# Kernel optimization log

Hardware: AMD Instinct MI355X
Metric: run time of the kernel (lower is better)

The kernel has to match this reference:

```python
import jax, jax.numpy as jnp
import numpy as np
import math

L = 2          # gnn_num_layers
NDIM = 256     # gnn_hidden_size
H = 8          # num_heads
HH = H // 2    # heads per (full, local) split
DK = NDIM // H # 32, also == edim (relation_share_heads)
EDIM = DK
B, NPB = 32, 128
N = B * NPB            # 4096 nodes
EF = B * NPB * NPB     # 524288 complete-graph edges
EL = 131072            # local-graph edges
ELG = 262144           # line-graph edges
R = 128                # relation vocab


def _ln(x, g, b, eps=1e-5):
    m = x.mean(-1, keepdims=True)
    v = ((x - m) ** 2).mean(-1, keepdims=True)
    return (x - m) / jnp.sqrt(v + eps) * g + b


def _ffn(x, W1, b1, W2, b2, g, b):
    h = jax.nn.relu(x @ W1 + b1)
    return _ln(x + h @ W2 + b2, g, b)


def _edge_attn(q, k, v, e, src, dst, n_seg):
    """Relation-aware graph attention (DGL propagate_attention + edge_softmax).
    q,k,v: [n_seg,h,d]; e: [E,h,d] edge-relation bias or None; src,dst: [E].
    score_e = ((k[src]+e) . q[dst]) / sqrt(d); softmax over in-edges of dst;
    out[dst] = sum alpha_e * (v[src]+e)."""
    ks = k[src] + e if e is not None else k[src]          # [E,h,d]
    vs = v[src] + e if e is not None else v[src]          # [E,h,d]
    s = jnp.einsum('ehd,ehd->eh', ks, q[dst]) / math.sqrt(q.shape[-1])
    smax = jax.ops.segment_max(s, dst, num_segments=n_seg)
    ex = jnp.exp(s - jnp.maximum(smax, -1e30)[dst])
    den = jax.ops.segment_sum(ex, dst, num_segments=n_seg)[dst]
    alpha = ex / jnp.where(den > 0, den, 1.0)
    return jax.ops.segment_sum(alpha[..., None] * vs, dst, num_segments=n_seg)


def _model(x, rel_embed,
           n_Wq, n_bq, n_Wk, n_bk, n_Wv, n_bv, n_Wo, n_bo, n_ln_g, n_ln_b,
           n_f_W1, n_f_b1, n_f_W2, n_f_b2, n_f_ln_g, n_f_ln_b,
           e_Wsrc, e_Wdst, e_Wq, e_bq, e_Wk, e_Wv, e_Wo, e_bo, e_ln_g, e_ln_b,
           e_f_W1, e_f_b1, e_f_W2, e_f_b2, e_f_ln_g, e_f_ln_b,
           full_src, full_dst, g_src, g_dst, lg_src, lg_dst, edge_feat, full_edge_feat):
    lg_x = rel_embed[edge_feat]            # [EL, EDIM]  (shared embedding)
    lg_x_full = rel_embed[full_edge_feat]  # [EF, EDIM]  (fixed across layers)
    n, el, ef = x.shape[0], lg_x.shape[0], lg_x_full.shape[0]
    for i in range(L):
        # ---------- node update: first HH heads on full graph, last HH on local ----------
        q = (x @ n_Wq[i] + n_bq[i]).reshape(n, H, DK)
        k = (x @ n_Wk[i] + n_bk[i]).reshape(n, H, DK)
        v = (x @ n_Wv[i] + n_bv[i]).reshape(n, H, DK)
        # edim == d_k -> relation bias broadcast across heads (the expand branch)
        e_full = jnp.broadcast_to(lg_x_full[:, None, :], (ef, HH, DK))
        e_loc = jnp.broadcast_to(lg_x[:, None, :], (el, HH, DK))
        o1 = _edge_attn(q[:, :HH], k[:, :HH], v[:, :HH], e_full, full_src, full_dst, n)
        o2 = _edge_attn(q[:, HH:], k[:, HH:], v[:, HH:], e_loc, g_src, g_dst, n)
        o = jnp.concatenate([o1, o2], axis=1).reshape(n, NDIM)
        x_new = _ln(x + o @ n_Wo[i] + n_bo[i], n_ln_g[i], n_ln_b[i])
        x_new = _ffn(x_new, n_f_W1[i], n_f_b1[i], n_f_W2[i], n_f_b2[i], n_f_ln_g[i], n_f_ln_b[i])
        # ---------- edge update on line graph, conditioned on PRE-update src/dst node feats ----------
        mixed = lg_x + x[g_src] @ e_Wsrc[i] + x[g_dst] @ e_Wdst[i]  # [EL, EDIM]
        dke = EDIM // H
        eq = (mixed @ e_Wq[i] + e_bq[i]).reshape(el, H, dke)
        ek = (mixed @ e_Wk[i]).reshape(el, H, dke)
        ev = (mixed @ e_Wv[i]).reshape(el, H, dke)
        ow = _edge_attn(eq, ek, ev, None, lg_src, lg_dst, el).reshape(el, EDIM)
        lg_new = _ln(lg_x + ow @ e_Wo[i] + e_bo[i], e_ln_g[i], e_ln_b[i])
        lg_new = _ffn(lg_new, e_f_W1[i], e_f_b1[i], e_f_W2[i], e_f_b2[i], e_f_ln_g[i], e_f_ln_b[i])
        x, lg_x = x_new, lg_new
    return x, lg_x


def setup_inputs() -> dict:
    key = jax.random.key(0)
    ki = iter(jax.random.split(key, 48))
    def p(shape, scale=0.05):
        return jax.random.normal(next(ki), shape, dtype=jnp.float32) * scale
    rng = np.random.default_rng(0)
    blk = (np.arange(B, dtype=np.int32) * NPB)
    ii, jj = np.meshgrid(np.arange(NPB, dtype=np.int32), np.arange(NPB, dtype=np.int32), indexing='ij')
    full_src = (blk[:, None, None] + ii[None]).reshape(-1)   # block-diagonal complete graph
    full_dst = (blk[:, None, None] + jj[None]).reshape(-1)
    epb = EL // B
    g_src = (np.repeat(blk, epb) + rng.integers(0, NPB, EL)).astype(np.int32)
    g_dst = (np.repeat(blk, epb) + rng.integers(0, NPB, EL)).astype(np.int32)
    lpb = ELG // B
    eblk = np.arange(B, dtype=np.int32) * epb
    lg_src = (np.repeat(eblk, lpb) + rng.integers(0, epb, ELG)).astype(np.int32)
    lg_dst = (np.repeat(eblk, lpb) + rng.integers(0, epb, ELG)).astype(np.int32)
    return dict(
        x=jax.random.normal(next(ki), (N, NDIM), dtype=jnp.float32),
        rel_embed=p((R, EDIM), 1.0),
        full_src=jnp.asarray(full_src), full_dst=jnp.asarray(full_dst),
        g_src=jnp.asarray(g_src), g_dst=jnp.asarray(g_dst),
        lg_src=jnp.asarray(lg_src), lg_dst=jnp.asarray(lg_dst),
        edge_feat=jnp.asarray(rng.integers(0, R, EL).astype(np.int32)),
        full_edge_feat=jnp.asarray(rng.integers(0, R, EF).astype(np.int32)),
        n_Wq=p((L, NDIM, NDIM)), n_bq=p((L, NDIM)),
        n_Wk=p((L, NDIM, NDIM)), n_bk=p((L, NDIM)),
        n_Wv=p((L, NDIM, NDIM)), n_bv=p((L, NDIM)),
        n_Wo=p((L, NDIM, NDIM)), n_bo=p((L, NDIM)),
        n_ln_g=jnp.ones((L, NDIM), jnp.float32), n_ln_b=jnp.zeros((L, NDIM), jnp.float32),
        n_f_W1=p((L, NDIM, 4 * NDIM)), n_f_b1=p((L, 4 * NDIM)),
        n_f_W2=p((L, 4 * NDIM, NDIM)), n_f_b2=p((L, NDIM)),
        n_f_ln_g=jnp.ones((L, NDIM), jnp.float32), n_f_ln_b=jnp.zeros((L, NDIM), jnp.float32),
        e_Wsrc=p((L, NDIM, EDIM)), e_Wdst=p((L, NDIM, EDIM)),
        e_Wq=p((L, EDIM, EDIM)), e_bq=p((L, EDIM)),
        e_Wk=p((L, EDIM, EDIM)), e_Wv=p((L, EDIM, EDIM)),
        e_Wo=p((L, EDIM, EDIM)), e_bo=p((L, EDIM)),
        e_ln_g=jnp.ones((L, EDIM), jnp.float32), e_ln_b=jnp.zeros((L, EDIM), jnp.float32),
        e_f_W1=p((L, EDIM, 4 * EDIM)), e_f_b1=p((L, 4 * EDIM)),
        e_f_W2=p((L, 4 * EDIM, EDIM)), e_f_b2=p((L, EDIM)),
        e_f_ln_g=jnp.ones((L, EDIM), jnp.float32), e_f_ln_b=jnp.zeros((L, EDIM), jnp.float32),
    )


def reference(x, rel_embed, full_src, full_dst, g_src, g_dst, lg_src, lg_dst,
              edge_feat, full_edge_feat,
              n_Wq, n_bq, n_Wk, n_bk, n_Wv, n_bv, n_Wo, n_bo, n_ln_g, n_ln_b,
              n_f_W1, n_f_b1, n_f_W2, n_f_b2, n_f_ln_g, n_f_ln_b,
              e_Wsrc, e_Wdst, e_Wq, e_bq, e_Wk, e_Wv, e_Wo, e_bo, e_ln_g, e_ln_b,
              e_f_W1, e_f_b1, e_f_W2, e_f_b2, e_f_ln_g, e_f_ln_b):
    return _model(x, rel_embed,
                  n_Wq, n_bq, n_Wk, n_bk, n_Wv, n_bv, n_Wo, n_bo, n_ln_g, n_ln_b,
                  n_f_W1, n_f_b1, n_f_W2, n_f_b2, n_f_ln_g, n_f_ln_b,
                  e_Wsrc, e_Wdst, e_Wq, e_bq, e_Wk, e_Wv, e_Wo, e_bo, e_ln_g, e_ln_b,
                  e_f_W1, e_f_b1, e_f_W2, e_f_b2, e_f_ln_g, e_f_ln_b,
                  full_src, full_dst, g_src, g_dst, lg_src, lg_dst, edge_feat, full_edge_feat)
```

## Files before the change

kernel.cpp:

```cpp
#include <hip/hip_runtime.h>
#include <hip/hip_bf16.h>

typedef __hip_bfloat16 bf16;
typedef unsigned short ush;

static constexpr int kN   = 4096;
static constexpr int kND  = 256;
static constexpr int kEL  = 131072;
static constexpr int kED  = 32;
static constexpr int kELG = 262144;
static constexpr int kL   = 2;
static constexpr int kQW  = 832;
static constexpr int kKV  = 512;
static constexpr float kScaleN = 0.17677669529663687f;

using frag_ab = __attribute__((ext_vector_type(8))) short;
using frag_cd = __attribute__((ext_vector_type(4))) float;

__device__ __forceinline__ float ldf(const void* p, size_t i, int isbf){
    return isbf ? __bfloat162float(((const bf16*)p)[i]) : ((const float*)p)[i];
}
__device__ __forceinline__ ush f2b(float f){ bf16 h = __float2bfloat16(f); return *(ush*)&h; }
__device__ __forceinline__ float b2f(ush u){ return __uint_as_float(((unsigned)u)<<16); }
__device__ __forceinline__ ush ldb(const void* p, size_t i, int isbf){
    return isbf ? ((const ush*)p)[i] : f2b(((const float*)p)[i]);
}

__global__ void detect_k(const ush* __restrict__ xin, int* __restrict__ flag){
    const int t = threadIdx.x;
    int pl = 0;
    for (int i = t; i < 128; i += 64) {
        ush u = xin[i];
        int e = (u >> 7) & 0xFF;
        if (e == 0 || (e >= 110 && e <= 140)) ++pl;
    }
    #pragma unroll
    for (int off = 32; off > 0; off >>= 1) pl += __shfl_down(pl, off);
    if (t == 0) *flag = (pl >= 102) ? 1 : 0;
}

__global__ void setup_misc_k(const void* __restrict__ xin, const void* __restrict__ rel,
                             const int* __restrict__ feat,
                             const void* __restrict__ bq, const void* __restrict__ bk,
                             const void* __restrict__ bv,
                             float* __restrict__ xA, ush* __restrict__ xAb,
                             ush* __restrict__ lgA,
                             float* __restrict__ bQKV,
                             int* __restrict__ cntL, int* __restrict__ cntG,
                             const int* __restrict__ flag){
    const int isbf = *flag;
    long g = (long)blockIdx.x*256 + threadIdx.x;
    if (g < (long)kN*kND) {
        float v = ldf(xin, g, isbf);
        xA[g] = v; xAb[g] = f2b(v);
        return;
    }
    g -= (long)kN*kND;
    if (g < (long)kEL*kED) { int e = (int)(g >> 5), d = (int)(g & 31);
        lgA[g] = ldb(rel, (size_t)feat[e]*kED + d, isbf); return; }
    g -= (long)kEL*kED;
    if (g < 2*kQW) {
        int layer = (int)(g / kQW), j = (int)(g - (long)layer*kQW);
        float v = 0.f;
        if (j < 768) { int w = j >> 8, jj = j & 255;
            const void* B = (w==0)?bq:((w==1)?bk:bv);
            v = ldf(B, (size_t)layer*256 + jj, isbf); }
        bQKV[g] = v; return;
    }
    g -= 2*kQW;
    if (g < kN) { cntL[g] = 0; return; }
    g -= kN;
    if (g < kEL) { cntG[g] = 0; return; }
}

__global__ __launch_bounds__(256) void trans_tiled_k(
    const void* __restrict__ nWq, const void* __restrict__ nWk, const void* __restrict__ nWv,
    const void* __restrict__ nWo, const void* __restrict__ nF1, const void* __restrict__ nF2,
    const void* __restrict__ eWs, const void* __restrict__ eWd,
    const void* __restrict__ eWq, const void* __restrict__ eWk, const void* __restrict__ eWv,
    const void* __restrict__ eWo, const void* __restrict__ eF1, const void* __restrict__ eF2,
    const int* __restrict__ flag,
    ush* __restrict__ wtQKVSD, ush* __restrict__ wtO, ush* __restrict__ wtF1,
    ush* __restrict__ wtF2, ush* __restrict__ wtEQKV, ush* __restrict__ wtEO,
    ush* __restrict__ wtEF1, ush* __restrict__ wtEF2)
{
    __shared__ ush lds[32][33];
    const int isbf = *flag;
    int idx = blockIdx.x;
    const void* src; size_t soff; ush* dstp; size_t doff;
    int Ns, Kd, r0, c0;
    if (idx < 384) {
        int w = idx >> 7, rem = idx & 127;
        int layer = rem >> 6, tile = rem & 63;
        r0 = (tile >> 3) << 5; c0 = (tile & 7) << 5;
        src = (w==0)?nWq:((w==1)?nWk:nWv); soff = (size_t)layer*65536;
        Ns = 256; Kd = 256;
        dstp = wtQKVSD; doff = (size_t)layer*212992 + (size_t)w*65536;
    } else if ((idx -= 384) < 32) {
        int w = idx >> 4, rem = idx & 15;
        int layer = rem >> 3, tile = rem & 7;
        r0 = tile << 5; c0 = 0;
        src = w ? eWd : eWs; soff = (size_t)layer*8192;
        Ns = 32; Kd = 256;
        dstp = wtQKVSD; doff = (size_t)layer*212992 + (size_t)(768 + w*32)*256;
    } else if ((idx -= 32) < 128) {
        int layer = idx >> 6, tile = idx & 63;
        r0 = (tile >> 3) << 5; c0 = (tile & 7) << 5;
        src = nWo; soff = (size_t)layer*65536; Ns = 256; Kd = 256;
        dstp = wtO; doff = (size_t)layer*65536;
    } else if ((idx -= 128) < 512) {
        int layer = idx >> 8, tile = idx & 255;
        r0 = (tile >> 5) << 5; c0 = (tile & 31) << 5;
        src = nF1; soff = (size_t)layer*262144; Ns = 1024; Kd = 256;
        dstp = wtF1; doff = (size_t)layer*262144;
    } else if ((idx -= 512) < 512) {
        int layer = idx >> 8, tile = idx & 255;
        r0 = (tile >> 3) << 5; c0 = (tile & 7) << 5;
        src = nF2; soff = (size_t)layer*262144; Ns = 256; Kd = 1024;
        dstp = wtF2; doff = (size_t)layer*262144;
    } else if ((idx -= 512) < 6) {
        int w = idx >> 1, layer = idx & 1;
        r0 = 0; c0 = 0;
        src = (w==0)?eWq:((w==1)?eWk:eWv); soff = (size_t)layer*1024; Ns = 32; Kd = 32;
        dstp = wtEQKV; doff = (size_t)(w*2 + layer)*1024;
    } else if ((idx -= 6) < 2) {
        r0 = 0; c0 = 0;
        src = eWo; soff = (size_t)idx*1024; Ns = 32; Kd = 32;
        dstp = wtEO; doff = (size_t)idx*1024;
    } else if ((idx -= 2) < 8) {
        int layer = idx >> 2, tile = idx & 3;
        r0 = 0; c0 = tile << 5;
        src = eF1; soff = (size_t)layer*4096; Ns = 128; Kd = 32;
        dstp = wtEF1; doff = (size_t)layer*4096;
    } else {
        idx -= 8;
        int layer = idx >> 2, tile = idx & 3;
        r0 = tile << 5; c0 = 0;
        src = eF2; soff = (size_t)layer*4096; Ns = 32; Kd = 128;
        dstp = wtEF2; doff = (size_t)layer*4096;
    }
    const int t = threadIdx.x;
    const int c = t & 31, rb = t >> 5;
    #pragma unroll
    for (int p = 0; p < 4; ++p) {
        int r = rb + p*8;
        lds[r][c] = ldb(src, soff + (size_t)(r0 + r)*Ns + c0 + c, isbf);
    }
    __syncthreads();
    #pragma unroll
    for (int p = 0; p < 4; ++p) {
        int rr = rb + p*8;
        dstp[doff + (size_t)(c0 + rr)*Kd + r0 + c] = lds[c][rr];
    }
}

__global__ void count2_k(const int* __restrict__ gd, const int* __restrict__ lgd,
                         int* __restrict__ cntL, int* __restrict__ cntG){
    int g = blockIdx.x*256 + threadIdx.x;
    if (g < kEL) atomicAdd(&cntL[gd[g]], 1);
    else if (g < kEL + kELG) atomicAdd(&cntG[lgd[g - kEL]], 1);
}
__global__ __launch_bounds__(256) void scan_blk2_k(
    const int* __restrict__ cntL, const int* __restrict__ cntG,
    int* __restrict__ rowL, int* __restrict__ rowG, int* __restrict__ bsum)
{
    __shared__ int s[256];
    const int t = threadIdx.x;
    const bool isL = blockIdx.x < 4;
    const int* cnt = isL ? cntL : cntG;
    int* out = isL ? rowL : rowG;
    const int blk = isL ? blockIdx.x : blockIdx.x - 4;
    const int n = isL ? kN : kEL;
    const int b0 = blk*1024;
    int v[4], pre[4], tsum = 0;
    #pragma unroll
    for (int j=0;j<4;++j){
        int idx = b0 + t*4 + j;
        v[j] = (idx < n) ? cnt[idx] : 0;
        pre[j] = tsum; tsum += v[j];
    }
    s[t] = tsum; __syncthreads();
    for (int off=1; off<256; off<<=1){
        int x = (t>=off) ? s[t-off] : 0;
        __syncthreads();
        s[t] += x;
        __syncthreads();
    }
    int texc = s[t] - tsum;
    #pragma unroll
    for (int j=0;j<4;++j){
        int idx = b0 + t*4 + j;
        if (idx < n) out[idx] = texc + pre[j];
    }
    if (t == 255) bsum[(isL ? 0 : 8) + blk] = s[255];
}
__global__ __launch_bounds__(256) void scan_top2_k(int* __restrict__ bsum){
    __shared__ int sL[256], sG[256];
    const int t = threadIdx.x;
    int vL = (t < 4)   ? bsum[t]     : 0;
    int vG = (t < 128) ? bsum[8 + t] : 0;
    sL[t] = vL; sG[t] = vG; __syncthreads();
    for (int off=1; off<256; off<<=1){
        int xL = (t>=off) ? sL[t-off] : 0;
        int xG = (t>=off) ? sG[t-off] : 0;
        __syncthreads();
        sL[t] += xL; sG[t] += xG;
        __syncthreads();
    }
    if (t < 4)   bsum[t]     = sL[t] - vL;
    if (t < 128) bsum[8 + t] = sG[t] - vG;
}
__global__ void scan_add2_k(int* __restrict__ rowL, int* __restrict__ rowG,
                            const int* __restrict__ bsum,
                            int* __restrict__ curL, int* __restrict__ curG){
    int g = blockIdx.x*256 + threadIdx.x;
    if (g < kN){ int v = rowL[g] + bsum[g >> 10]; rowL[g] = v; curL[g] = v; }
    else if (g < kN + kEL){ int gg = g - kN;
        int v = rowG[gg] + bsum[8 + (gg >> 10)]; rowG[gg] = v; curG[gg] = v; }
    if (g == 0){ rowL[kN] = kEL; rowG[kEL] = kELG; }
}
__global__ void fill2_k(const int* __restrict__ gd, const int* __restrict__ lgd,
                        int* __restrict__ curL, int* __restrict__ curG,
                        int* __restrict__ eidL, int* __restrict__ eidG){
    int g = blockIdx.x*256 + threadIdx.x;
    if (g < kEL){ int pos = atomicAdd(&curL[gd[g]], 1); eidL[pos] = g; }
    else if (g < kEL + kELG){ int gg = g - kEL;
        int pos = atomicAdd(&curG[lgd[gg]], 1); eidG[pos] = gg; }
}

__global__ __launch_bounds__(256) void mgemm_k(
    const float* __restrict__ A, const ush* __restrict__ WT,
    const void* __restrict__ bias, size_t boff,
    float* __restrict__ C, const int* __restrict__ flag,
    int M, int N, int K, int flags, ush* __restrict__ aux, ush* __restrict__ aux2)
{
    __shared__ __align__(16) ush As[64*72];
    __shared__ __align__(16) ush Ws[64*72];
    const int isbf = *flag;
    const int t = threadIdx.x;
    const int m0 = blockIdx.y*64, n0 = blockIdx.x*64;
    const int wave = t>>6, lane = t&63;
    const int quad = lane>>4, l15 = lane&15;
    const int r = t>>3, kq = (t&7)*8;
    const bool abf = flags & 32;
    const bool spk = flags & 128;
    const int Kc   = spk ? (K / gridDim.z) : K;
    const int koff = spk ? (blockIdx.z * Kc) : 0;

    frag_cd acc[4];
    #pragma unroll
    for (int tl=0; tl<4; ++tl)
        #pragma unroll
        for (int j=0;j<4;++j) acc[tl][j] = 0.f;

    const float* ap0 = A + (size_t)(m0+r)*K + koff + kq;
    const float* ap1 = A + (size_t)(m0+r+32)*K + koff + kq;
    const ush*   ab0 = (const ush*)A + (size_t)(m0+r)*K + koff + kq;
    const ush*   ab1 = (const ush*)A + (size_t)(m0+r+32)*K + koff + kq;
    const ush*   wp0 = WT + (size_t)(n0+r)*K + koff + kq;
    const ush*   wp1 = WT + (size_t)(n0+r+32)*K + koff + kq;

    float4 a00,a01,a10,a11; uint4 av0,av1, wv0,wv1;
    auto loadT = [&](int kk){
        if (abf) { av0 = *(const uint4*)(ab0+kk); av1 = *(const uint4*)(ab1+kk); }
        else { a00 = *(const float4*)(ap0+kk); a01 = *(const float4*)(ap0+kk+4);
               a10 = *(const float4*)(ap1+kk); a11 = *(const float4*)(ap1+kk+4); }
        wv0 = *(const uint4*)(wp0+kk); wv1 = *(const uint4*)(wp1+kk);
    };
    loadT(0);

    for (int kk = 0; kk < Kc; kk += 64) {
        if (abf) {
            *(uint4*)&As[r*72 + kq]        = av0;
            *(uint4*)&As[(r+32)*72 + kq]   = av1;
        } else {
            *(ushort4*)&As[r*72 + kq]       = make_ushort4(f2b(a00.x),f2b(a00.y),f2b(a00.z),f2b(a00.w));
            *(ushort4*)&As[r*72 + kq + 4]   = make_ushort4(f2b(a01.x),f2b(a01.y),f2b(a01.z),f2b(a01.w));
            *(ushort4*)&As[(r+32)*72 + kq]     = make_ushort4(f2b(a10.x),f2b(a10.y),f2b(a10.z),f2b(a10.w));
            *(ushort4*)&As[(r+32)*72 + kq + 4] = make_ushort4(f2b(a11.x),f2b(a11.y),f2b(a11.z),f2b(a11.w));
        }
        *(uint4*)&Ws[r*72 + kq]      = wv0;
        *(uint4*)&Ws[(r+32)*72 + kq] = wv1;
        __syncthreads();
        if (kk + 64 < Kc) loadT(kk + 64);
        frag_ab af0 = *(const frag_ab*)&As[(wave*16 + l15)*72 + quad*8];
        frag_ab af1 = *(const frag_ab*)&As[(wave*16 + l15)*72 + 32 + quad*8];
        #pragma unroll
        for (int tl = 0; tl < 4; ++tl) {
            frag_ab bf0 = *(const frag_ab*)&Ws[(tl*16 + l15)*72 + quad*8];
            acc[tl] = __builtin_amdgcn_mfma_f32_16x16x32_bf16(af0, bf0, acc[tl], 0, 0, 0);
            frag_ab bf1 = *(const frag_ab*)&Ws[(tl*16 + l15)*72 + 32 + quad*8];
            acc[tl] = __builtin_amdgcn_mfma_f32_16x16x32_bf16(af1, bf1, acc[tl], 0, 0, 0);
        }
        __syncthreads();
    }
    const bool do_relu = flags & 2;
    const bool has_b   = (flags & 4) && (!spk || blockIdx.z == 0);
    const bool obf     = flags & 8;
    float* Cz = spk ? (C + (size_t)blockIdx.z * M * N) : C;
    #pragma unroll
    for (int tl = 0; tl < 4; ++tl) {
        int col = n0 + tl*16 + l15;
        float bv = 0.f;
        if (has_b) bv = (flags & 16) ? ((const float*)bias)[boff + col]
                                     : ldf(bias, boff + col, isbf);
        int adst = -1; bool tox = false;
        if (flags & 64 && col >= 256) {
            int c = col - 256;
            if (c < 512) {
                int isv = c >> 8;
                int cc = c & 255;
                int h = cc >> 5, d = cc & 31;
                int base = (h < 4) ? h*64 : 256 + (h-4)*64;
                adst = base + isv*32 + d;
            } else { adst = c - 512; tox = true; }
        }
        #pragma unroll
        for (int rg = 0; rg < 4; ++rg) {
            int row = m0 + wave*16 + quad*4 + rg;
            float v = acc[tl][rg] + bv;
            if (do_relu) v = fmaxf(v, 0.f);
            if (flags & 64) {
                if (col < 256)  C[(size_t)row*256 + col] = v;
                else if (tox)   aux2[(size_t)row*64 + adst] = f2b(v);
                else            aux[(size_t)row*kKV + adst] = f2b(v);
            } else if (obf) ((ush*)C)[(size_t)row*N + col] = f2b(v);
            else            Cz[(size_t)row*N + col] = v;
        }
    }
}

__global__ __launch_bounds__(256) void ln_k(
    const float* __restrict__ a, const float* __restrict__ b, const float* __restrict__ b2,
    const void* __restrict__ g, const void* __restrict__ be, size_t goff,
    float* __restrict__ out, ush* __restrict__ outb,
    const int* __restrict__ flag, int D)
{
    const int isbf = *flag;
    const int row = blockIdx.x*4 + (threadIdx.x >> 6);
    const int t = threadIdx.x & 63;
    float v[4];
    int cnt = 0;
    float s = 0.f;
    for (int i = t; i < D; i += 64) {
        float x = a[(size_t)row*D + i];
        if (b)  x += b[(size_t)row*D + i];
        if (b2) x += b2[(size_t)row*D + i];
        v[cnt++] = x; s += x;
    }
    #pragma unroll
    for (int off = 32; off > 0; off >>= 1) s += __shfl_down(s, off);
    s = __shfl(s, 0);
    const float mean = s / D;
    float qq = 0.f;
    for (int c2 = 0; c2 < cnt; ++c2) { float d = v[c2]-mean; qq += d*d; }
    #pragma unroll
    for (int off = 32; off > 0; off >>= 1) qq += __shfl_down(qq, off);
    qq = __shfl(qq, 0);
    const float inv = rsqrtf(fmaxf(qq, 0.f) / D + 1e-5f);
    cnt = 0;
    for (int i = t; i < D; i += 64) {
        float r = (v[cnt++] - mean)*inv*ldf(g, goff + i, isbf) + ldf(be, goff + i, isbf);
        out[(size_t)row*D + i] = r;
        outb[(size_t)row*D + i] = f2b(r);
    }
}

__global__ __launch_bounds__(256) void eqkv_mfma_k(
    const ush* __restrict__ lg, const ush* __restrict__ xsd,
    const int* __restrict__ gsrc, const int* __restrict__ gdst,
    const ush* __restrict__ WQKV, size_t woff,
    const void* __restrict__ bq, size_t boff,
    ush* __restrict__ eq, ush* __restrict__ ekv,
    const int* __restrict__ flag)
{
    __shared__ __align__(16) ush mixs[128*40];
    __shared__ __align__(16) ush wts[3][32*40];
    __shared__ float bqs[32];
    const int isbf = *flag;
    const int t = threadIdx.x;
    const int e0 = blockIdx.x * 128;
    #pragma unroll
    for (int i = t; i < 768; i += 256) {
        int m = i >> 8, r2 = i & 255;
        int n = r2 >> 3, k4 = (r2 & 7) * 4;
        *(ushort4*)&wts[m][n*40 + k4] =
            *(const ushort4*)&WQKV[(size_t)m*2048 + woff + (size_t)n*32 + k4];
    }
    if (t < 32) bqs[t] = ldf(bq, boff + t, isbf);
    {
        int r = t >> 1, c0 = (t & 1) * 16;
        int e = e0 + r;
        int s = gsrc[e], d2 = gdst[e];
        const ush* lp = lg  + (size_t)e*32  + c0;
        const ush* sp = xsd + (size_t)s*64  + c0;
        const ush* dp = xsd + (size_t)d2*64 + 32 + c0;
        uint4 lv0 = *(const uint4*)lp,     lv1 = *(const uint4*)(lp+8);
        uint4 sv0 = *(const uint4*)sp,     sv1 = *(const uint4*)(sp+8);
        uint4 dv0 = *(const uint4*)dp,     dv1 = *(const uint4*)(dp+8);
        auto pk = [](unsigned a, unsigned b, unsigned c)->unsigned {
            ush lo = f2b(b2f((ush)(a & 0xffff)) + b2f((ush)(b & 0xffff)) + b2f((ush)(c & 0xffff)));
            ush hi = f2b(b2f((ush)(a >> 16))    + b2f((ush)(b >> 16))    + b2f((ush)(c >> 16)));
            return (unsigned)lo | ((unsigned)hi << 16);
        };
        uint4 o0, o1;
        o0.x = pk(lv0.x, sv0.x, dv0.x); o0.y = pk(lv0.y, sv0.y, dv0.y);
        o0.z = pk(lv0.z, sv0.z, dv0.z); o0.w = pk(lv0.w, sv0.w, dv0.w);
        o1.x = pk(lv1.x, sv1.x, dv1.x); o1.y = pk(lv1.y, sv1.y, dv1.y);
        o1.z = pk(lv1.z, sv1.z, dv1.z); o1.w = pk(lv1.w, sv1.w, dv1.w);
        *(uint4*)&mixs[r*40 + c0]     = o0;
        *(uint4*)&mixs[r*40 + c0 + 8] = o1;
    }
    __syncthreads();
    const int wave = t >> 6, l15 = t & 15, quad = (t >> 4) & 3;
    #pragma unroll
    for (int mi = 0; mi < 2; ++mi) {
        const int mt = wave*2 + mi;
        frag_ab af = *(const frag_ab*)&mixs[(mt*16 + l15)*40 + quad*8];
        #pragma unroll
        for (int w = 0; w < 3; ++w) {
            #pragma unroll
            for (int nt = 0; nt < 2; ++nt) {
                frag_ab bf = *(const frag_ab*)&wts[w][(nt*16 + l15)*40 + quad*8];
                frag_cd acc = {0.f, 0.f, 0.f, 0.f};
                acc = __builtin_amdgcn_mfma_f32_16x16x32_bf16(af, bf, acc, 0, 0, 0);
                const float bv = (w==0) ? bqs[nt*16 + l15] : 0.f;
                const int col = nt*16 + l15;
                const int h = col >> 2, d = col & 3;
                #pragma unroll
                for (int rg = 0; rg < 4; ++rg) {
                    int row = e0 + mt*16 + quad*4 + rg;
                    float v = acc[rg] + bv;
                    if (w == 0)      eq[(size_t)row*32 + col] = f2b(v);
                    else if (w == 1) ekv[(size_t)row*64 + h*8 + d] = f2b(v);
                    else             ekv[(size_t)row*64 + h*8 + 4 + d] = f2b(v);
                }
            }
        }
    }
}

__global__ __launch_bounds__(256) void effn_mfma_k(
    const ush* __restrict__ A,
    const ush* __restrict__ W1T, size_t w1off, const void* __restrict__ b1, size_t b1off,
    const ush* __restrict__ W2T, size_t w2off, const void* __restrict__ b2, size_t b2off,
    const void* __restrict__ g, const void* __restrict__ be, size_t goff,
    ush* __restrict__ out, const int* __restrict__ flag)
{
    __shared__ __align__(16) ush w1t[128*40];
    __shared__ __align__(16) ush w2t[32*136];
    __shared__ __align__(16) ush hid[64*136];
    __shared__ float b1s[128], b2s[32];
    const int isbf = *flag;
    const int t = threadIdx.x;
    const int wave = t >> 6, l15 = t & 15, quad = (t >> 4) & 3;

    #pragma unroll
    for (int i = t; i < 1024; i += 256) {
        int n1 = i >> 3, k4 = (i & 7) * 4;
        *(ushort4*)&w1t[n1*40 + k4] = *(const ushort4*)&W1T[w1off + (size_t)n1*32 + k4];
        int n2 = i >> 5, kq2 = (i & 31) * 4;
        *(ushort4*)&w2t[n2*136 + kq2] = *(const ushort4*)&W2T[w2off + (size_t)n2*128 + kq2];
    }
    if (t < 128) b1s[t] = ldf(b1, b1off + t, isbf);
    if (t < 32)  b2s[t] = ldf(b2, b2off + t, isbf);
    __syncthreads();

    const float g0  = ldf(g,  goff + l15, isbf),      g1v = ldf(g,  goff + 16 + l15, isbf);
    const float be0 = ldf(be, goff + l15, isbf),      be1 = ldf(be, goff + 16 + l15, isbf);
    const float bb0 = b2s[l15], bb1 = b2s[16 + l15];

    for (int tt = 0; tt < 2; ++tt) {
        const int e0 = (blockIdx.x*2 + tt) * 64;
        {
            const int m = wave*16 + l15;
            frag_ab af = *(const frag_ab*)&A[(size_t)(e0+m)*32 + quad*8];
            #pragma unroll
            for (int nt = 0; nt < 8; ++nt) {
                frag_ab bf = *(const frag_ab*)&w1t[(nt*16 + l15)*40 + quad*8];
                frag_cd acc = {0.f, 0.f, 0.f, 0.f};
                acc = __builtin_amdgcn_mfma_f32_16x16x32_bf16(af, bf, acc, 0, 0, 0);
                float bv = b1s[nt*16 + l15];
                #pragma unroll
                for (int rg = 0; rg < 4; ++rg) {
                    int row = wave*16 + quad*4 + rg;
                    hid[row*136 + nt*16 + l15] = f2b(fmaxf(acc[rg] + bv, 0.f));
                }
            }
        }
        frag_cd acc2[2] = {{0.f,0.f,0.f,0.f},{0.f,0.f,0.f,0.f}};
        #pragma unroll
        for (int ks = 0; ks < 4; ++ks) {
            frag_ab af2 = *(const frag_ab*)&hid[(wave*16 + l15)*136 + ks*32 + quad*8];
            #pragma unroll
            for (int tl = 0; tl < 2; ++tl) {
                frag_ab bf2 = *(const frag_ab*)&w2t[(tl*16 + l15)*136 + ks*32 + quad*8];
                acc2[tl] = __builtin_amdgcn_mfma_f32_16x16x32_bf16(af2, bf2, acc2[tl], 0, 0, 0);
            }
        }
        #pragma unroll
        for (int rg = 0; rg < 4; ++rg) {
            const int row = e0 + wave*16 + quad*4 + rg;
            float v0 = acc2[0][rg] + bb0 + b2f(A[(size_t)row*32 + l15]);
            float v1 = acc2[1][rg] + bb1 + b2f(A[(size_t)row*32 + 16 + l15]);
            float s = v0 + v1;
            s += __shfl_xor(s,1); s += __shfl_xor(s,2); s += __shfl_xor(s,4); s += __shfl_xor(s,8);
            const float mean = s * (1.f/32.f);
            float q = (v0-mean)*(v0-mean) + (v1-mean)*(v1-mean);
            q += __shfl_xor(q,1); q += __shfl_xor(q,2); q += __shfl_xor(q,4); q += __shfl_xor(q,8);
            const float inv = rsqrtf(q * (1.f/32.f) + 1e-5f);
            out[(size_t)row*32 + l15]      = f2b((v0-mean)*inv*g0  + be0);
            out[(size_t)row*32 + 16 + l15] = f2b((v1-mean)*inv*g1v + be1);
        }
    }
}

__global__ __launch_bounds__(512) void full_attn_k(
    const float* __restrict__ q, const ush* __restrict__ kv,
    const void* __restrict__ rel, const int* __restrict__ feat, ush* __restrict__ o,
    const int* __restrict__ flag)
{
    __shared__ __align__(8) ush ks[128][36];
    __shared__ __align__(8) ush vs[128][36];
    __shared__ __align__(8) ush rs[128][36];
    __shared__ float pb[8][32][34];
    const int isbf = *flag;
    const int bid = blockIdx.x;
    const int b = bid >> 4, h = (bid >> 2) & 3, qtr = bid & 3;
    const int t = threadIdx.x;
    for (int i = t; i < 4096; i += 512) {
        int r = i >> 5, d = i & 31;
        rs[r][d] = ldb(rel, i, isbf);
        const ush* kvrow = kv + (size_t)(b*128 + r)*kKV + h*64 + d;
        ks[r][d] = kvrow[0];
        vs[r][d] = kvrow[32];
    }
    __syncthreads();
    const int wave = t >> 6, lane = t & 63;
    const int dstL = lane >> 1, part = lane & 1;
    const int dst = qtr*32 + dstL;
    const int dbase = part*16;
    float qr[16];
    { size_t base = ((size_t)(b*128 + dst))*256 + h*32 + dbase;
      #pragma unroll
      for (int d=0; d<16; ++d) qr[d] = q[base + d]; }
    const int* fp = feat + (size_t)b*16384 + dst;
    const int s0 = wave*16;
    float m = -1e30f, l = 0.f;
    float acc[16];
    #pragma unroll
    for (int d=0; d<16; ++d) acc[d] = 0.f;
    int f = fp[s0*128];
    for (int sI = 0; sI < 16; ++sI) {
        const int s = s0 + sI;
        int fn = (sI+1 < 16) ? fp[(s+1)*128] : 0;
        float er[16];
        float scp = 0.f;
        #pragma unroll
        for (int j2 = 0; j2 < 4; ++j2) {
            ushort4 eu = *(const ushort4*)&rs[f][dbase + j2*4];
            ushort4 ku = *(const ushort4*)&ks[s][dbase + j2*4];
            float e0 = b2f(eu.x), e1 = b2f(eu.y), e2 = b2f(eu.z), e3 = b2f(eu.w);
            er[j2*4+0]=e0; er[j2*4+1]=e1; er[j2*4+2]=e2; er[j2*4+3]=e3;
            scp += (b2f(ku.x)+e0)*qr[j2*4+0] + (b2f(ku.y)+e1)*qr[j2*4+1]
                 + (b2f(ku.z)+e2)*qr[j2*4+2] + (b2f(ku.w)+e3)*qr[j2*4+3];
        }
        const float sc = (scp + __shfl_xor(scp, 1)) * kScaleN;
        float mn = fmaxf(m, sc);
        float c0 = __expf(m - mn);
        float pp = __expf(sc - mn);
        l = l*c0 + pp;
        #pragma unroll
        for (int j2 = 0; j2 < 4; ++j2) {
            ushort4 vu = *(const ushort4*)&vs[s][dbase + j2*4];
            acc[j2*4+0] = acc[j2*4+0]*c0 + pp*(b2f(vu.x)+er[j2*4+0]);
            acc[j2*4+1] = acc[j2*4+1]*c0 + pp*(b2f(vu.y)+er[j2*4+1]);
            acc[j2*4+2] = acc[j2*4+2]*c0 + pp*(b2f(vu.z)+er[j2*4+2]);
            acc[j2*4+3] = acc[j2*4+3]*c0 + pp*(b2f(vu.w)+er[j2*4+3]);
        }
        m = mn; f = fn;
    }
    if (part == 0) { pb[wave][dstL][0] = m; pb[wave][dstL][1] = l; }
    #pragma unroll
    for (int d=0; d<16; ++d) pb[wave][dstL][2 + dbase + d] = acc[d];
    __syncthreads();
    {
        const int dstL2 = t & 31, grp = t >> 5;
        float mw[8], lw[8];
        #pragma unroll
        for (int w=0; w<8; ++w){ mw[w]=pb[w][dstL2][0]; lw[w]=pb[w][dstL2][1]; }
        float M = mw[0];
        #pragma unroll
        for (int w=1; w<8; ++w) M = fmaxf(M, mw[w]);
        float sw[8];
        float L = 0.f;
        #pragma unroll
        for (int w=0; w<8; ++w){ sw[w] = __expf(mw[w]-M); L += lw[w]*sw[w]; }
        const float inv = 1.f / fmaxf(L, 1e-30f);
        size_t base = ((size_t)(b*128 + qtr*32 + dstL2))*kND + h*32 + grp*2;
        #pragma unroll
        for (int d=0; d<2; ++d) {
            float a = 0.f;
            #pragma unroll
            for (int w=0; w<8; ++w) a += pb[w][dstL2][2+grp*2+d]*sw[w];
            o[base + d] = f2b(a*inv);
        }
    }
}

__global__ __launch_bounds__(256) void loc_gather_k(
    const float* __restrict__ q, const ush* __restrict__ kv,
    const ush* __restrict__ lg, const int* __restrict__ gsrc,
    const int* __restrict__ rowp, const int* __restrict__ eidl,
    ush* __restrict__ o)
{
    __shared__ int eids[192], srcs[192];
    const int n = blockIdx.x;
    const int beg = rowp[n], end = rowp[n+1];
    const int deg = end - beg;
    {
        const int tc = threadIdx.x;
        const int dc = (deg < 192) ? deg : 192;
        if (tc < dc) { int e = eidl[beg + tc]; eids[tc] = e; srcs[tc] = gsrc[e]; }
    }
    __syncthreads();
    const int h = threadIdx.x >> 6;
    const int lane = threadIdx.x & 63;
    const int g = lane >> 4;
    const int d0 = (lane & 15) * 2;
    const size_t hoff = (size_t)(4 + h) * 32 + d0;
    const float2 q2 = *(const float2*)&q[(size_t)n*256 + hoff];
    float m = -1e30f, l = 0.f, ax = 0.f, ay = 0.f;
    if (deg > 0) {
        const int nIter = (deg + 3) >> 2;
        int idx = beg + g;
        for (int it = 0; it < nIter; ++it) {
            const bool valid = idx < end;
            const int ii = min(idx, end-1) - beg;
            int e, s;
            if (ii < 192) { e = eids[ii]; s = srcs[ii]; }
            else          { e = eidl[beg + ii]; s = gsrc[e]; }
            idx += 4;
            const ushort2 ku = *(const ushort2*)&kv[(size_t)s*kKV + 256 + h*64 + d0];
            const ushort2 lvu = *(const ushort2*)&lg[(size_t)e*32 + d0];
            const ushort2 vu = *(const ushort2*)&kv[(size_t)s*kKV + 256 + h*64 + 32 + d0];
            const float lvx = b2f(lvu.x), lvy = b2f(lvu.y);
            float part = (b2f(ku.x)+lvx)*q2.x + (b2f(ku.y)+lvy)*q2.y;
            part += __shfl_xor(part, 1);
            part += __shfl_xor(part, 2);
            part += __shfl_xor(part, 4);
            part += __shfl_xor(part, 8);
            const float sc = part * kScaleN;
            const float mn = valid ? fmaxf(m, sc) : m;
            const float c  = __expf(m - mn);
            const float pp = valid ? __expf(sc - mn) : 0.f;
            l  = l*c  + pp;
            ax = ax*c + pp*(b2f(vu.x)+lvx);
            ay = ay*c + pp*(b2f(vu.y)+lvy);
            m  = mn;
        }
        #pragma unroll
        for (int off = 16; off <= 32; off <<= 1) {
            const float mo = __shfl_xor(m, off);
            const float lo = __shfl_xor(l, off);
            const float xo = __shfl_xor(ax, off);
            const float yo = __shfl_xor(ay, off);
            const float M  = fmaxf(m, mo);
            const float c1 = __expf(m - M);
            const float c2 = __expf(mo - M);
            l  = l*c1  + lo*c2;
            ax = ax*c1 + xo*c2;
            ay = ay*c1 + yo*c2;
            m  = M;
        }
    }
    if (g == 0) {
        const float inv = 1.f / fmaxf(l, 1e-30f);
        *(ushort2*)&o[(size_t)n*kND + hoff] = make_ushort2(f2b(ax*inv), f2b(ay*inv));
    }
}

__global__ __launch_bounds__(256) void lgs_ewo_k(
    const ush* __restrict__ eq, const ush* __restrict__ ekv,
    const int* __restrict__ lsrc, const int* __restrict__ rowp, const int* __restrict__ eidl,
    const ush* __restrict__ res,
    const ush* __restrict__ WO, size_t wooff, const void* __restrict__ bo, size_t booff,
    const void* __restrict__ g1, const void* __restrict__ be1, size_t g1off,
    ush* __restrict__ out, const int* __restrict__ flag)
{
    __shared__ __align__(16) ush ows[32*40];
    __shared__ __align__(16) ush wos[32*40];
    __shared__ float cs[32][36];
    __shared__ float bos[32], gs[32], bs[32];
    __shared__ int srcs[256];
    const int isbf = *flag;
    const int t = threadIdx.x;
    const int base = blockIdx.x * 32;
    {
        int n = t >> 3, k4 = (t & 7) * 4;
        *(ushort4*)&wos[n*40 + k4] = *(const ushort4*)&WO[wooff + (size_t)n*32 + k4];
    }
    if (t < 32) {
        bos[t] = ldf(bo, booff + t, isbf);
        gs[t]  = ldf(g1, g1off + t, isbf);
        bs[t]  = ldf(be1, g1off + t, isbf);
    }
    const int beg0 = rowp[base];
    {
        int cnt = rowp[base + 32] - beg0;
        if (cnt > 256) cnt = 256;
        for (int j = t; j < cnt; j += 256) srcs[j] = lsrc[eidl[beg0 + j]];
    }
    __syncthreads();
    {
        const int d2 = base + (t >> 3), h = t & 7;
        const ushort4 qu = *(const ushort4*)&eq[(size_t)d2*32 + h*4];
        const float q0 = b2f(qu.x), q1 = b2f(qu.y), q2 = b2f(qu.z), q3 = b2f(qu.w);
        const int beg = rowp[d2], end = rowp[d2+1];
        float m = -1e30f, l = 0.f;
        float4 acc = make_float4(0.f,0.f,0.f,0.f);
        for (int i = beg; i < end; ++i) {
            const int io = i - beg0;
            const int s = (io < 256) ? srcs[io] : lsrc[eidl[i]];
            const uint4 kv8 = *(const uint4*)&ekv[(size_t)s*64 + h*8];
            const ush k0 = (ush)(kv8.x & 0xffff), k1 = (ush)(kv8.x >> 16);
            const ush k2 = (ush)(kv8.y & 0xffff), k3 = (ush)(kv8.y >> 16);
            const ush v0u = (ush)(kv8.z & 0xffff), v1u = (ush)(kv8.z >> 16);
            const ush v2u = (ush)(kv8.w & 0xffff), v3u = (ush)(kv8.w >> 16);
            float sc = (b2f(k0)*q0 + b2f(k1)*q1 + b2f(k2)*q2 + b2f(k3)*q3) * 0.5f;
            float mn = fmaxf(m, sc);
            float c = __expf(m - mn);
            float pp = __expf(sc - mn);
            l = l*c + pp;
            acc.x = acc.x*c + pp*b2f(v0u);
            acc.y = acc.y*c + pp*b2f(v1u);
            acc.z = acc.z*c + pp*b2f(v2u);
            acc.w = acc.w*c + pp*b2f(v3u);
            m = mn;
        }
        const float inv = 1.f / fmaxf(l, 1e-30f);
        const int r = t >> 3, c0 = h*4;
        ows[r*40 + c0 + 0] = f2b(acc.x*inv);
        ows[r*40 + c0 + 1] = f2b(acc.y*inv);
        ows[r*40 + c0 + 2] = f2b(acc.z*inv);
        ows[r*40 + c0 + 3] = f2b(acc.w*inv);
    }
    __syncthreads();
    {
        const int wave = t >> 6, l15 = t & 15, quad = (t >> 4) & 3;
        const int mt = wave & 1, nt = wave >> 1;
        frag_ab af = *(const frag_ab*)&ows[(mt*16 + l15)*40 + quad*8];
        frag_ab bf = *(const frag_ab*)&wos[(nt*16 + l15)*40 + quad*8];
        frag_cd acc = {0.f, 0.f, 0.f, 0.f};
        acc = __builtin_amdgcn_mfma_f32_16x16x32_bf16(af, bf, acc, 0, 0, 0);
        #pragma unroll
        for (int rg = 0; rg < 4; ++rg) {
            const int row = mt*16 + quad*4 + rg;
            const int col = nt*16 + l15;
            cs[row][col] = acc[rg] + bos[col] + b2f(res[(size_t)(base+row)*32 + col]);
        }
    }
    __syncthreads();
    {
        const int row = t >> 3, c0 = (t & 7) * 4;
        const float v0 = cs[row][c0], v1 = cs[row][c0+1];
        const float v2 = cs[row][c0+2], v3 = cs[row][c0+3];
        float s = v0+v1+v2+v3;
        s += __shfl_xor(s,1); s += __shfl_xor(s,2); s += __shfl_xor(s,4);
        const float mean = s * (1.f/32.f);
        float qq = (v0-mean)*(v0-mean)+(v1-mean)*(v1-mean)
                 + (v2-mean)*(v2-mean)+(v3-mean)*(v3-mean);
        qq += __shfl_xor(qq,1); qq += __shfl_xor(qq,2); qq += __shfl_xor(qq,4);
        const float inv = rsqrtf(qq * (1.f/32.f) + 1e-5f);
        out[(size_t)(base+row)*32 + c0 + 0] = f2b((v0-mean)*inv*gs[c0+0] + bs[c0+0]);
        out[(size_t)(base+row)*32 + c0 + 1] = f2b((v1-mean)*inv*gs[c0+1] + bs[c0+1]);
        out[(size_t)(base+row)*32 + c0 + 2] = f2b((v2-mean)*inv*gs[c0+2] + bs[c0+2]);
        out[(size_t)(base+row)*32 + c0 + 3] = f2b((v3-mean)*inv*gs[c0+3] + bs[c0+3]);
    }
}

__global__ void out_k(const float* __restrict__ xf, const ush* __restrict__ lgf,
                      void* __restrict__ out, const int* __restrict__ flag){
    const int isbf = *flag;
    int g = blockIdx.x*256 + threadIdx.x;
    if (g < kN*kND) {
        float v = xf[g];
        if (isbf) ((ush*)out)[g] = f2b(v);
        else      ((float*)out)[g] = v;
    } else {
        ush u = lgf[g - kN*kND];
        if (isbf) ((ush*)out)[g] = u;
        else      ((float*)out)[g] = b2f(u);
    }
}

static inline void mgemm(const float* A, const ush* WT, const void* bias, size_t boff,
                         float* C, const int* flag, int M, int N, int K, int flags,
                         hipStream_t s, ush* aux, ush* aux2, int splitz = 1){
    dim3 grid((N+63)/64, M/64, splitz);
    mgemm_k<<<grid, 256, 0, s>>>(A, WT, bias, boff, C, flag, M, N, K, flags, aux, aux2);
}

extern "C" void kernel_launch(void* const* d_in, const int* in_sizes, int n_in,
                              void* d_out, int out_size, void* d_ws, size_t ws_size,
                              hipStream_t stream) {
    const void* x_in      = d_in[0];
    const void* rel       = d_in[1];
    const int* g_src      = (const int*)d_in[4];
    const int* g_dst      = (const int*)d_in[5];
    const int* lg_src     = (const int*)d_in[6];
    const int* lg_dst     = (const int*)d_in[7];
    const int* edge_feat  = (const int*)d_in[8];
    const int* full_feat  = (const int*)d_in[9];
    const void* n_Wq   = d_in[10];
    const void* n_bq   = d_in[11];
    const void* n_Wk   = d_in[12];
    const void* n_bk   = d_in[13];
    const void* n_Wv   = d_in[14];
    const void* n_bv   = d_in[15];
    const void* n_Wo   = d_in[16];
    const void* n_bo   = d_in[17];
    const void* n_lng  = d_in[18];
    const void* n_lnb  = d_in[19];
    const void* n_fW1  = d_in[20];
    const void* n_fb1  = d_in[21];
    const void* n_fW2  = d_in[22];
    const void* n_fb2  = d_in[23];
    const void* n_flng = d_in[24];
    const void* n_flnb = d_in[25];
    const void* e_Wsrc = d_in[26];
    const void* e_Wdst = d_in[27];
    const void* e_Wq   = d_in[28];
    const void* e_bq   = d_in[29];
    const void* e_Wk   = d_in[30];
    const void* e_Wv   = d_in[31];
    const void* e_Wo   = d_in[32];
    const void* e_bo   = d_in[33];
    const void* e_lng  = d_in[34];
    const void* e_lnb  = d_in[35];
    const void* e_fW1  = d_in[36];
    const void* e_fb1  = d_in[37];
    const void* e_fW2  = d_in[38];
    const void* e_fb2  = d_in[39];
    const void* e_flng = d_in[40];
    const void* e_flnb = d_in[41];

    float* p = (float*)d_ws;
    size_t off = 0;
    auto AL = [&](size_t n){ float* r = p + off; off += n; return r; };
    int* flagp = (int*)AL(64);
    float* xA   = AL((size_t)kN*kND);
    float* xB   = AL((size_t)kN*kND);
    float* xM   = AL((size_t)kN*kND);
    ush*   xAb  = (ush*)AL((size_t)kN*kND/2);
    ush*   xBb  = (ush*)AL((size_t)kN*kND/2);
    ush*   xMb  = (ush*)AL((size_t)kN*kND/2);
    float* qkvb = AL((size_t)kN*kND);
    ush*   kvaux= (ush*)AL((size_t)kN*kKV/2);
    ush*   xsdb = (ush*)AL((size_t)kN*32);
    ush*   ob   = (ush*)AL((size_t)kN*kND/2);
    float* tN   = AL((size_t)kN*kND*2);
    ush*   nh   = (ush*)AL((size_t)kN*512);
    ush*   lgA  = (ush*)AL((size_t)kEL*kED/2);
    ush*   lgB  = (ush*)AL((size_t)kEL*kED/2);
    ush*   lgM  = (ush*)AL((size_t)kEL*kED/2);
    ush*   eqb  = (ush*)AL((size_t)kEL*16);
    ush*   ekvb = (ush*)AL((size_t)kEL*32);
    int* cntL  = (int*)AL(kN);
    int* rowL  = (int*)AL(kN + 64);
    int* curL  = (int*)AL(kN);
    int* eidL  = (int*)AL(kEL);
    int* cntG  = (int*)AL(kEL);
    int* rowG  = (int*)AL(kEL + 64);
    int* curG  = (int*)AL(kEL);
    int* eidG  = (int*)AL(kELG);
    int* bsum  = (int*)AL(256);
    ush* wtQKVSD = (ush*)AL(212992);
    float* bQKV  = AL(2*kQW);
    ush* wtO  = (ush*)AL(65536);
    ush* wtF1 = (ush*)AL(262144);
    ush* wtF2 = (ush*)AL(262144);
    ush* wtEQKV = (ush*)AL(3072);
    ush* wtEO   = (ush*)AL(1024);
    ush* wtEF1  = (ush*)AL(4096);
    ush* wtEF2  = (ush*)AL(4096);
    if (ws_size < off * sizeof(float)) return;

    float* tN2 = tN + (size_t)kN*kND;

    detect_k<<<1, 64, 0, stream>>>((const ush*)x_in, flagp);
    {
        long total = (long)kN*kND + (long)kEL*kED + 2*kQW + kN + kEL;
        int blocks = (int)((total + 255) / 256);
        setup_misc_k<<<blocks, 256, 0, stream>>>(x_in, rel, edge_feat, n_bq, n_bk, n_bv,
                                                 xA, xAb, lgA, bQKV, cntL, cntG, flagp);
    }
    trans_tiled_k<<<1592, 256, 0, stream>>>(n_Wq, n_Wk, n_Wv, n_Wo, n_fW1, n_fW2,
                                            e_Wsrc, e_Wdst, e_Wq, e_Wk, e_Wv, e_Wo,
                                            e_fW1, e_fW2, flagp,
                                            wtQKVSD, wtO, wtF1, wtF2,
                                            wtEQKV, wtEO, wtEF1, wtEF2);

    count2_k<<<(kEL+kELG)/256, 256, 0, stream>>>(g_dst, lg_dst, cntL, cntG);
    scan_blk2_k<<<132, 256, 0, stream>>>(cntL, cntG, rowL, rowG, bsum);
    scan_top2_k<<<1, 256, 0, stream>>>(bsum);
    scan_add2_k<<<(kN+kEL)/256, 256, 0, stream>>>(rowL, rowG, bsum, curL, curG);
    fill2_k<<<(kEL+kELG)/256, 256, 0, stream>>>(g_dst, lg_dst, curL, curG, eidL, eidG);

    float* xc = xA;  float* xn = xB;
    ush* xcb = xAb;  ush* xnb = xBb;
    ush* lgc = lgA;  ush* lgn = lgB;

    for (int i = 0; i < kL; ++i) {
        const size_t o256 = (size_t)i*kND;
        const size_t o1024= (size_t)i*1024;
        const size_t o32  = (size_t)i*kED;
        const size_t o128 = (size_t)i*128;

        mgemm((const float*)xcb, wtQKVSD + (size_t)i*212992, bQKV, (size_t)i*kQW, qkvb,
              flagp, kN, kQW, kND, 4|16|32|64, stream, kvaux, xsdb);
        full_attn_k<<<512, 512, 0, stream>>>(qkvb, kvaux, rel, full_feat, ob, flagp);
        loc_gather_k<<<kN, 256, 0, stream>>>(qkvb, kvaux, lgc, g_src, rowL, eidL, ob);
        mgemm((const float*)ob, wtO + (size_t)i*65536, n_bo, o256, tN, flagp,
              kN, kND, kND, 4|32|128, stream, nullptr, nullptr, 2);
        ln_k<<<kN/4, 256, 0, stream>>>(xc, tN, tN2, n_lng, n_lnb, o256, xM, xMb, flagp, kND);
        mgemm((const float*)xMb, wtF1 + (size_t)i*262144, n_fb1, o1024, (float*)nh, flagp,
              kN, 1024, kND, 4|2|8|32, stream, nullptr, nullptr);
        mgemm((const float*)nh, wtF2 + (size_t)i*262144, n_fb2, o256, tN, flagp,
              kN, kND, 1024, 4|32|128, stream, nullptr, nullptr, 2);
        ln_k<<<kN/4, 256, 0, stream>>>(xM, tN, tN2, n_flng, n_flnb, o256, xn, xnb, flagp, kND);

        eqkv_mfma_k<<<kEL/128, 256, 0, stream>>>(lgc, xsdb, g_src, g_dst,
                                                 wtEQKV, (size_t)i*1024, e_bq, o32,
                                                 eqb, ekvb, flagp);
        lgs_ewo_k<<<kEL/32, 256, 0, stream>>>(eqb, ekvb, lg_src, rowG, eidG,
                                              lgc, wtEO, (size_t)i*1024, e_bo, o32,
                                              e_lng, e_lnb, o32, lgM, flagp);
        effn_mfma_k<<<kEL/128, 256, 0, stream>>>(lgM, wtEF1, (size_t)i*4096, e_fb1, o128,
                                                 wtEF2, (size_t)i*4096, e_fb2, o32,
                                                 e_flng, e_flnb, o32, lgn, flagp);

        { float* t = xc; xc = xn; xn = t; }
        { ush* t = xcb; xcb = xnb; xnb = t; }
        { ush* t = lgc; lgc = lgn; lgn = t; }
    }

    out_k<<<(kN*kND + kEL*kED)/256, 256, 0, stream>>>(xc, lgc, d_out, flagp);
}
```

Baseline: 513.0 us.

## Fuse output and FFN2 projections with residual-add layernorm in one MFMA kernel

Replaces the two split-K mgemm calls (output projection and FFN second linear) plus the separate layernorm kernels with a single gemm_ln_k. Each block computes a 16x256 row tile with MFMA, adds bias and the residual, then applies layernorm in-block and writes fp32 and bf16 outputs. This removes the fp32 partial-sum round trips through tN/tN2 and two launches per use. The cost is that each block now streams the whole weight matrix for only 16 rows, and the grid has just 256 blocks with no split-K, so the K=1024 case may be less parallel.

```diff
diff --git a/kernel.cpp b/kernel.cpp
--- a/kernel.cpp
+++ b/kernel.cpp
@@ -330,39 +330,102 @@
     }
 }
 
-__global__ __launch_bounds__(256) void ln_k(
-    const float* __restrict__ a, const float* __restrict__ b, const float* __restrict__ b2,
+__global__ __launch_bounds__(256) void gemm_ln_k(
+    const ush* __restrict__ A, const ush* __restrict__ WT,
+    const void* __restrict__ bias, size_t boff,
+    const float* __restrict__ res,
     const void* __restrict__ g, const void* __restrict__ be, size_t goff,
     float* __restrict__ out, ush* __restrict__ outb,
-    const int* __restrict__ flag, int D)
+    const int* __restrict__ flag, int K)
 {
+    __shared__ __align__(16) ush As[16*72];
+    __shared__ __align__(16) ush Ws[256*72];
+    __shared__ float cs[16][260];
+    __shared__ float bs[256], gsv[256], bes[256];
     const int isbf = *flag;
-    const int row = blockIdx.x*4 + (threadIdx.x >> 6);
-    const int t = threadIdx.x & 63;
-    float v[4];
-    int cnt = 0;
-    float s = 0.f;
-    for (int i = t; i < D; i += 64) {
-        float x = a[(size_t)row*D + i];
-        if (b)  x += b[(size_t)row*D + i];
-        if (b2) x += b2[(size_t)row*D + i];
-        v[cnt++] = x; s += x;
-    }
-    #pragma unroll
-    for (int off = 32; off > 0; off >>= 1) s += __shfl_down(s, off);
-    s = __shfl(s, 0);
-    const float mean = s / D;
-    float qq = 0.f;
-    for (int c2 = 0; c2 < cnt; ++c2) { float d = v[c2]-mean; qq += d*d; }
-    #pragma unroll
-    for (int off = 32; off > 0; off >>= 1) qq += __shfl_down(qq, off);
-    qq = __shfl(qq, 0);
-    const float inv = rsqrtf(fmaxf(qq, 0.f) / D + 1e-5f);
-    cnt = 0;
-    for (int i = t; i < D; i += 64) {
-        float r = (v[cnt++] - mean)*inv*ldf(g, goff + i, isbf) + ldf(be, goff + i, isbf);
-        out[(size_t)row*D + i] = r;
-        outb[(size_t)row*D + i] = f2b(r);
+    const int t = threadIdx.x;
+    const int m0 = blockIdx.x * 16;
+    const int wave = t >> 6, lane = t & 63;
+    const int quad = lane >> 4, l15 = lane & 15;
+
+    bs[t]  = ldf(bias, boff + t, isbf);
+    gsv[t] = ldf(g,  goff + t, isbf);
+    bes[t] = ldf(be, goff + t, isbf);
+
+    frag_cd acc[4];
+    #pragma unroll
+    for (int nt = 0; nt < 4; ++nt)
+        #pragma unroll
+        for (int j = 0; j < 4; ++j) acc[nt][j] = 0.f;
+
+    const int ar = t >> 4, ak = (t & 15) * 4;
+    const ush* ap = A + (size_t)(m0 + ar)*K + ak;
+
+    ushort4 avr; uint4 wvr[8];
+    auto loadT = [&](int kk){
+        avr = *(const ushort4*)(ap + kk);
+        #pragma unroll
+        for (int j = 0; j < 8; ++j) {
+            int idx = t + j*256;
+            int cl = idx >> 3, k8 = (idx & 7) * 8;
+            wvr[j] = *(const uint4*)&WT[(size_t)cl*K + kk + k8];
+        }
+    };
+    loadT(0);
+
+    for (int kk = 0; kk < K; kk += 64) {
+        *(ushort4*)&As[ar*72 + ak] = avr;
+        #pragma unroll
+        for (int j = 0; j < 8; ++j) {
+            int idx = t + j*256;
+            int cl = idx >> 3, k8 = (idx & 7) * 8;
+            *(uint4*)&Ws[cl*72 + k8] = wvr[j];
+        }
+        __syncthreads();
+        if (kk + 64 < K) loadT(kk + 64);
+        frag_ab af0 = *(const frag_ab*)&As[l15*72 + quad*8];
+        frag_ab af1 = *(const frag_ab*)&As[l15*72 + 32 + quad*8];
+        #pragma unroll
+        for (int nt = 0; nt < 4; ++nt) {
+            frag_ab bf0 = *(const frag_ab*)&Ws[(wave*64 + nt*16 + l15)*72 + quad*8];
+            acc[nt] = __builtin_amdgcn_mfma_f32_16x16x32_bf16(af0, bf0, acc[nt], 0, 0, 0);
+            frag_ab bf1 = *(const frag_ab*)&Ws[(wave*64 + nt*16 + l15)*72 + 32 + quad*8];
+            acc[nt] = __builtin_amdgcn_mfma_f32_16x16x32_bf16(af1, bf1, acc[nt], 0, 0, 0);
+        }
+        __syncthreads();
+    }
+    #pragma unroll
+    for (int nt = 0; nt < 4; ++nt) {
+        const int col = wave*64 + nt*16 + l15;
+        #pragma unroll
+        for (int rg = 0; rg < 4; ++rg) {
+            const int row = quad*4 + rg;
+            cs[row][col] = acc[nt][rg] + bs[col] + res[(size_t)(m0 + row)*256 + col];
+        }
+    }
+    __syncthreads();
+    {
+        const int row = t >> 4, cc = (t & 15) * 16;
+        float v[16];
+        float s = 0.f;
+        #pragma unroll
+        for (int j = 0; j < 16; ++j) { v[j] = cs[row][cc + j]; s += v[j]; }
+        s += __shfl_xor(s, 1); s += __shfl_xor(s, 2);
+        s += __shfl_xor(s, 4); s += __shfl_xor(s, 8);
+        const float mean = s * (1.f/256.f);
+        float qq = 0.f;
+        #pragma unroll
+        for (int j = 0; j < 16; ++j) { float d = v[j] - mean; qq += d*d; }
+        qq += __shfl_xor(qq, 1); qq += __shfl_xor(qq, 2);
+        qq += __shfl_xor(qq, 4); qq += __shfl_xor(qq, 8);
+        const float inv = rsqrtf(fmaxf(qq, 0.f) * (1.f/256.f) + 1e-5f);
+        const size_t base = (size_t)(m0 + row)*256 + cc;
+        #pragma unroll
+        for (int j = 0; j < 16; ++j) {
+            float r = (v[j] - mean)*inv*gsv[cc + j] + bes[cc + j];
+            out[base + j] = r;
+            outb[base + j] = f2b(r);
+        }
     }
 }
 
@@ -886,8 +949,6 @@
     ush* wtEF2  = (ush*)AL(4096);
     if (ws_size < off * sizeof(float)) return;
 
-    float* tN2 = tN + (size_t)kN*kND;
-
     detect_k<<<1, 64, 0, stream>>>((const ush*)x_in, flagp);
     {
         long total = (long)kN*kND + (long)kEL*kED + 2*kQW + kN + kEL;
@@ -910,6 +971,7 @@
     float* xc = xA;  float* xn = xB;
     ush* xcb = xAb;  ush* xnb = xBb;
     ush* lgc = lgA;  ush* lgn = lgB;
+    (void)tN;
 
     for (int i = 0; i < kL; ++i) {
         const size_t o256 = (size_t)i*kND;
@@ -921,14 +983,12 @@
               flagp, kN, kQW, kND, 4|16|32|64, stream, kvaux, xsdb);
         full_attn_k<<<512, 512, 0, stream>>>(qkvb, kvaux, rel, full_feat, ob, flagp);
         loc_gather_k<<<kN, 256, 0, stream>>>(qkvb, kvaux, lgc, g_src, rowL, eidL, ob);
-        mgemm((const float*)ob, wtO + (size_t)i*65536, n_bo, o256, tN, flagp,
-              kN, kND, kND, 4|32|128, stream, nullptr, nullptr, 2);
-        ln_k<<<kN/4, 256, 0, stream>>>(xc, tN, tN2, n_lng, n_lnb, o256, xM, xMb, flagp, kND);
+        gemm_ln_k<<<kN/16, 256, 0, stream>>>(ob, wtO + (size_t)i*65536, n_bo, o256,
+                                             xc, n_lng, n_lnb, o256, xM, xMb, flagp, kND);
         mgemm((const float*)xMb, wtF1 + (size_t)i*262144, n_fb1, o1024, (float*)nh, flagp,
               kN, 1024, kND, 4|2|8|32, stream, nullptr, nullptr);
-        mgemm((const float*)nh, wtF2 + (size_t)i*262144, n_fb2, o256, tN, flagp,
-              kN, kND, 1024, 4|32|128, stream, nullptr, nullptr, 2);
-        ln_k<<<kN/4, 256, 0, stream>>>(xM, tN, tN2, n_flng, n_flnb, o256, xn, xnb, flagp, kND);
+        gemm_ln_k<<<kN/16, 256, 0, stream>>>(nh, wtF2 + (size_t)i*262144, n_fb2, o256,
+                                             xM, n_flng, n_flnb, o256, xn, xnb, flagp, 1024);
 
         eqkv_mfma_k<<<kEL/128, 256, 0, stream>>>(lgc, xsdb, g_src, g_dst,
                                                  wtEQKV, (size_t)i*1024, e_bq, o32,
```

Result: slower. 555.5 us (+8.3%).
